# Kernel optimization log

Measured on AMD Instinct MI355X. Metric: run time of the kernel, lower is better.

The kernel has to match this reference:

```python
import jax, jax.numpy as jnp
import numpy as np

N_QUBIT = 22
N_LAYERS = 2
D_LOGICAL = 2  # num_logical_dim (one logical qubit)
DIM = 2 ** N_QUBIT


def _apply_ry(psi, th, q):
    # psi: (B, 2^n) complex64; Ry(th) on qubit q (q=0 is the most significant bit)
    half = th * 0.5
    c = jnp.cos(half).astype(jnp.complex64)
    s = jnp.sin(half).astype(jnp.complex64)
    psi4 = psi.reshape(psi.shape[0], 2 ** q, 2, -1)
    p0, p1 = psi4[:, :, 0], psi4[:, :, 1]
    out = jnp.stack([c * p0 - s * p1, s * p0 + c * p1], axis=2)
    return out.reshape(psi.shape)


def _apply_cnot(psi, c, t):
    a, b = (c, t) if c < t else (t, c)
    right = 2 ** (N_QUBIT - b - 1)
    mid = 2 ** (b - a - 1)
    psi6 = psi.reshape(psi.shape[0], 2 ** a, 2, mid, 2, right)
    if c < t:
        # control is axis 2; flip target axis 4 where control==1
        psi6 = psi6.at[:, :, 1, :, :, :].set(psi6[:, :, 1, :, ::-1, :])
    else:
        # control is axis 4; flip target axis 2 where control==1
        psi6 = psi6.at[:, :, :, :, 1, :].set(psi6[:, :, ::-1, :, 1, :])
    return psi6.reshape(psi.shape)


def _apply_pauli(psi, p, q):
    psi4 = psi.reshape(psi.shape[0], 2 ** q, 2, -1)
    p0, p1 = psi4[:, :, 0], psi4[:, :, 1]
    if p == 'X':
        out = jnp.stack([p1, p0], axis=2)
    elif p == 'Y':
        out = jnp.stack([-1j * p1, 1j * p0], axis=2)
    else:  # Z
        out = jnp.stack([p0, -p1], axis=2)
    return out.reshape(psi.shape)


def _encode(theta):
    # q0[i, i] = 1 for the logical basis states, then run the circuit
    psi = jnp.zeros((D_LOGICAL, DIM), jnp.complex64)
    psi = psi.at[jnp.arange(D_LOGICAL), jnp.arange(D_LOGICAL)].set(1.0)
    for l in range(N_LAYERS):
        for q in range(N_QUBIT):
            psi = _apply_ry(psi, theta[l, q], q)
        for q in range(N_QUBIT):
            psi = _apply_cnot(psi, q, (q + 1) % N_QUBIT)
    return psi


def _kl_loss(theta):
    psi = _encode(theta)  # (D_LOGICAL, 2^n)
    # Knill-Laflamme inner products T_e[i,j] = <psi_i| E_e |psi_j> for all weight-1 Paulis
    Ts = []
    for q in range(N_QUBIT):
        for p in ('X', 'Y', 'Z'):
            epsi = _apply_pauli(psi, p, q)
            Ts.append(jnp.einsum('is,js->ij', psi.conj(), epsi))
    T = jnp.stack(Ts)  # (3*N_QUBIT, D_LOGICAL, D_LOGICAL)
    diag = jnp.diagonal(T, axis1=1, axis2=2)
    lam = diag.mean(axis=1)  # per-error lambda_e
    res = T - lam[:, None, None] * jnp.eye(D_LOGICAL, dtype=T.dtype)
    # loss_type == 'L2'
    return jnp.sum(jnp.abs(res) ** 2)


def setup_inputs() -> dict:
    key = jax.random.key(0)
    theta = jax.random.normal(key, (N_LAYERS, N_QUBIT), dtype=jnp.float32)
    return {"theta": theta}


def reference(theta):
    return _kl_loss(theta)
```

## Files before the change

### kernel.cpp

```cpp
#include <hip/hip_runtime.h>

#define NQ 22
#define DIMN (1u << NQ)

struct MaskSet {
    unsigned L[NQ];
    unsigned Linv[NQ];
    unsigned xm[NQ];
    unsigned zm[NQ];
    unsigned frowHi[5];
};

constexpr MaskSet buildMasks() {
    MaskSet M{};
    for (int b = 0; b < NQ; ++b) M.L[b] = 1u << b;
    for (int q = 0; q < NQ; ++q) {
        int bc = NQ - 1 - q, bt = NQ - 1 - ((q + 1) % NQ);
        M.L[bt] ^= M.L[bc];
    }
    unsigned mat[NQ] = {}, aug[NQ] = {};
    for (int b = 0; b < NQ; ++b) { mat[b] = M.L[b]; aug[b] = 1u << b; }
    for (int col = 0; col < NQ; ++col) {
        int piv = col;
        while (!((mat[piv] >> col) & 1u)) ++piv;
        unsigned tm = mat[piv]; mat[piv] = mat[col]; mat[col] = tm;
        unsigned ta = aug[piv]; aug[piv] = aug[col]; aug[col] = ta;
        for (int r = 0; r < NQ; ++r)
            if (r != col && ((mat[r] >> col) & 1u)) { mat[r] ^= mat[col]; aug[r] ^= aug[col]; }
    }
    for (int b = 0; b < NQ; ++b) M.Linv[b] = aug[b];
    for (int j = 0; j < NQ; ++j) {
        int b = NQ - 1 - j;
        unsigned xmv = 0;
        for (int r = 0; r < NQ; ++r)
            if ((aug[r] >> b) & 1u) xmv |= 1u << r;
        M.xm[j] = xmv;
        M.zm[j] = M.L[b];
    }
    for (int j = 0; j < 5; ++j) {
        unsigned f = 0;
        for (int r = 0; r < NQ; ++r)
            if ((aug[r] >> (17 + j)) & 1u) f |= 1u << r;
        M.frowHi[j] = f;
    }
    return M;
}
constexpr int topbit_c(unsigned v) { int b = 0; while (v >> (b + 1)) ++b; return b; }
constexpr unsigned unionHi() {
    MaskSet M = buildMasks();
    unsigned u = 0;
    for (int j = 0; j < 5; ++j) u |= M.frowHi[j];
    return u;
}
static_assert((unionHi() & 0xFFFFu) == 0, "frowHi must only touch bits 16..21");

__device__ __forceinline__ float wave_sum(float v) {
    v += __shfl_down(v, 32); v += __shfl_down(v, 16); v += __shfl_down(v, 8);
    v += __shfl_down(v, 4);  v += __shfl_down(v, 2);  v += __shfl_down(v, 1);
    return v;
}
__device__ __forceinline__ float fflip(float v, unsigned sbit31) {
    return __int_as_float(__float_as_int(v) ^ (int)sbit31);
}
__device__ __forceinline__ unsigned ph4(unsigned g) { return g ^ ((g >> 6) & 3u); }

__global__ __launch_bounds__(256) void k_prep(const float* __restrict__ theta,
                                              float* __restrict__ acc,
                                              float* __restrict__ trig) {
    int t = threadIdx.x;
    acc[t] = 0.f;
    if (t < 2 * NQ) {
        int l = t / NQ, q = t % NQ, b = NQ - 1 - q;
        float h = 0.5f * theta[t];
        trig[l * 2 * NQ + b]      = cosf(h);
        trig[l * 2 * NQ + NQ + b] = sinf(h);
    }
}

__global__ __launch_bounds__(256, 1) void k_genHi(float* __restrict__ phi,
                                                  const float* __restrict__ trig,
                                                  float* __restrict__ acc) {
    constexpr MaskSet M = buildMasks();
    __shared__ float red[4 * 12];
    unsigned base = blockIdx.x * 256u + threadIdx.x;
    unsigned P0 = 0;
#pragma unroll
    for (int b = 0; b < NQ; ++b)
        P0 |= ((unsigned)__popc(base & M.Linv[b]) & 1u) << b;
    float pc = 1.f;
#pragma unroll
    for (int b = 1; b < 16; ++b) {
        float cvb = trig[b], svb = trig[NQ + b];
        pc *= ((P0 >> b) & 1u) ? svb : cvb;
    }
    float cv0 = trig[0], sv0 = trig[NQ];
    float C0 = pc * ((P0 & 1u) ? sv0 : cv0);
    float C1 = pc * ((P0 & 1u) ? cv0 : -sv0);
    float cb[6], sb[6];
#pragma unroll
    for (int k = 0; k < 6; ++k) { cb[k] = trig[16 + k]; sb[k] = trig[NQ + 16 + k]; }
    unsigned u0 = P0 >> 16;
    float v0[32], v1[32];
#pragma unroll
    for (int e = 0; e < 32; ++e) {
        unsigned F = 0;
        if (e & 1)  F ^= M.frowHi[0];
        if (e & 2)  F ^= M.frowHi[1];
        if (e & 4)  F ^= M.frowHi[2];
        if (e & 8)  F ^= M.frowHi[3];
        if (e & 16) F ^= M.frowHi[4];
        unsigned u = u0 ^ (F >> 16);
        float vp = (u & 1u) ? sb[0] : cb[0];
#pragma unroll
        for (int k = 1; k < 6; ++k) vp *= ((u >> k) & 1u) ? sb[k] : cb[k];
        v0[e] = vp * C0;
        v1[e] = vp * C1;
    }
    float c2[5], s2[5];
#pragma unroll
    for (int j = 0; j < 5; ++j) {
        c2[j] = trig[2 * NQ + 17 + j];
        s2[j] = trig[3 * NQ + 17 + j];
    }
#pragma unroll
    for (int j = 0; j < 5; ++j) {
#pragma unroll
        for (int e = 0; e < 32; ++e) {
            if (!(e & (1 << j))) {
                int e1 = e | (1 << j);
                float a0 = v0[e], a1 = v0[e1];
                v0[e]  = c2[j] * a0 - s2[j] * a1;
                v0[e1] = s2[j] * a0 + c2[j] * a1;
                float b0 = v1[e], b1 = v1[e1];
                v1[e]  = c2[j] * b0 - s2[j] * b1;
                v1[e1] = s2[j] * b0 + c2[j] * b1;
            }
        }
    }
#pragma unroll
    for (int e = 0; e < 32; ++e) {
        unsigned a = base | ((unsigned)e << 17);
        phi[a] = v0[e];
        phi[DIMN + a] = v1[e];
    }
    int lane = threadIdx.x & 63, w = threadIdx.x >> 6;
#pragma unroll
    for (int i = 1; i <= 3; ++i) {
        unsigned ex  = M.xm[i] >> 17;
        unsigned zme = M.zm[i] >> 17;
        float t00 = 0.f, t11 = 0.f, t01 = 0.f, u01 = 0.f;
#pragma unroll
        for (int e = 0; e < 32; ++e) {
            int ep = e ^ (int)ex;
            t00 += v0[e] * v0[ep];
            t11 += v1[e] * v1[ep];
            float p = v0[e] * v1[ep];
            t01 += p;
            unsigned sg = ((unsigned)__popc((unsigned)ep & zme) & 1u) << 31;
            u01 += fflip(p, sg);
        }
        float vals[4] = { t00, t11, t01, u01 };
#pragma unroll
        for (int j = 0; j < 4; ++j) {
            float v = wave_sum(vals[j]);
            if (lane == 0) red[w * 12 + (i - 1) * 4 + j] = v;
        }
    }
    __syncthreads();
    int t = threadIdx.x;
    if (t < 12) {
        float r = red[t] + red[12 + t] + red[24 + t] + red[36 + t];
        atomicAdd(&acc[4 + t], r);
    }
}

__global__ __launch_bounds__(256, 1) void k_midA(float* __restrict__ phi,
                                                 const float* __restrict__ trig,
                                                 float* __restrict__ acc) {
    constexpr MaskSet M = buildMasks();
    __shared__ float red[4 * 16];
    unsigned tid = blockIdx.x * 256u + threadIdx.x;
    unsigned base = (tid & 0xFFFu) | ((tid >> 12) << 17);
    float v0[32], v1[32];
#pragma unroll
    for (int e = 0; e < 32; ++e) {
        unsigned a = base | ((unsigned)e << 12);
        v0[e] = phi[a];
        v1[e] = phi[DIMN + a];
    }
    float c[5], s[5];
#pragma unroll
    for (int j = 0; j < 5; ++j) {
        c[j] = trig[2 * NQ + 12 + j];
        s[j] = trig[3 * NQ + 12 + j];
    }
#pragma unroll
    for (int j = 0; j < 5; ++j) {
#pragma unroll
        for (int e = 0; e < 32; ++e) {
            if (!(e & (1 << j))) {
                int e1 = e | (1 << j);
                float a0 = v0[e], a1 = v0[e1];
                v0[e]  = c[j] * a0 - s[j] * a1;
                v0[e1] = s[j] * a0 + c[j] * a1;
                float b0 = v1[e], b1 = v1[e1];
                v1[e]  = c[j] * b0 - s[j] * b1;
                v1[e1] = s[j] * b0 + c[j] * b1;
            }
        }
    }
#pragma unroll
    for (int e = 0; e < 32; ++e) {
        unsigned a = base | ((unsigned)e << 12);
        phi[a] = v0[e];
        phi[DIMN + a] = v1[e];
    }
    int lane = threadIdx.x & 63, w = threadIdx.x >> 6;
#pragma unroll
    for (int i = 5; i <= 8; ++i) {
        unsigned ex  = (M.xm[i] >> 12) & 31u;
        unsigned zme = (M.zm[i] >> 12) & 31u;
        unsigned bs31 = ((unsigned)__popc(base & M.zm[i]) & 1u) << 31;
        float t00 = 0.f, t11 = 0.f, t01 = 0.f, u01 = 0.f;
#pragma unroll
        for (int e = 0; e < 32; ++e) {
            int ep = e ^ (int)ex;
            t00 += v0[e] * v0[ep];
            t11 += v1[e] * v1[ep];
            float p = v0[e] * v1[ep];
            t01 += p;
            unsigned sg = ((unsigned)__popc((unsigned)ep & zme) & 1u) << 31;
            u01 += fflip(p, sg ^ bs31);
        }
        float vals[4] = { t00, t11, t01, u01 };
#pragma unroll
        for (int j = 0; j < 4; ++j) {
            float v = wave_sum(vals[j]);
            if (lane == 0) red[w * 16 + (i - 5) * 4 + j] = v;
        }
    }
    __syncthreads();
    int t = threadIdx.x;
    if (t < 16) {
        float r = red[t] + red[16 + t] + red[32 + t] + red[48 + t];
        atomicAdd(&acc[20 + t], r);
    }
}

__global__ __launch_bounds__(256) void k_low(float* __restrict__ phi,
                                             const float* __restrict__ trig,
                                             float* __restrict__ acc) {
    constexpr MaskSet M = buildMasks();
    __shared__ float As[4096];
    __shared__ float Bs[4096];
    __shared__ float red[4 * 44];
    float4* As4 = (float4*)As;
    float4* Bs4 = (float4*)Bs;
    int t = threadIdx.x;
    unsigned base = blockIdx.x * 4096u;
    float a[16], b[16];

    {
        const float4* g0 = (const float4*)(phi + base);
        const float4* g1 = (const float4*)(phi + DIMN + base);
#pragma unroll
        for (int k = 0; k < 4; ++k) {
            float4 va = g0[4 * t + k];
            a[4 * k] = va.x; a[4 * k + 1] = va.y; a[4 * k + 2] = va.z; a[4 * k + 3] = va.w;
            float4 vb = g1[4 * t + k];
            b[4 * k] = vb.x; b[4 * k + 1] = vb.y; b[4 * k + 2] = vb.z; b[4 * k + 3] = vb.w;
        }
#pragma unroll
        for (int g = 0; g < 4; ++g) {
            float c = trig[2 * NQ + g], s = trig[3 * NQ + g];
#pragma unroll
            for (int e = 0; e < 16; ++e) {
                if (!(e & (1 << g))) {
                    int e1 = e | (1 << g);
                    float x0 = a[e], x1 = a[e1];
                    a[e] = c * x0 - s * x1; a[e1] = s * x0 + c * x1;
                    float y0 = b[e], y1 = b[e1];
                    b[e] = c * y0 - s * y1; b[e1] = s * y0 + c * y1;
                }
            }
        }
        unsigned sw = (unsigned)(t >> 4) & 3u;
#pragma unroll
        for (int k = 0; k < 4; ++k) {
            unsigned f = ((unsigned)(4 * t + k)) ^ sw;
            As4[f] = make_float4(a[4 * k], a[4 * k + 1], a[4 * k + 2], a[4 * k + 3]);
            Bs4[f] = make_float4(b[4 * k], b[4 * k + 1], b[4 * k + 2], b[4 * k + 3]);
        }
    }
    __syncthreads();

    {
        unsigned lo = (unsigned)t & 15u, hi = (unsigned)t >> 4;
        unsigned swz = (hi & 3u) << 2;
#pragma unroll
        for (int j = 0; j < 16; ++j) {
            unsigned i = lo | ((unsigned)j << 4) | (hi << 8);
            a[j] = As[i ^ swz];
            b[j] = Bs[i ^ swz];
        }
#pragma unroll
        for (int g = 0; g < 4; ++g) {
            float c = trig[2 * NQ + 4 + g], s = trig[3 * NQ + 4 + g];
#pragma unroll
            for (int e = 0; e < 16; ++e) {
                if (!(e & (1 << g))) {
                    int e1 = e | (1 << g);
                    float x0 = a[e], x1 = a[e1];
                    a[e] = c * x0 - s * x1; a[e1] = s * x0 + c * x1;
                    float y0 = b[e], y1 = b[e1];
                    b[e] = c * y0 - s * y1; b[e1] = s * y0 + c * y1;
                }
            }
        }
#pragma unroll
        for (int j = 0; j < 16; ++j) {
            unsigned i = lo | ((unsigned)j << 4) | (hi << 8);
            As[i ^ swz] = a[j];
            Bs[i ^ swz] = b[j];
        }
    }
    __syncthreads();

    {
#pragma unroll
        for (int j = 0; j < 16; ++j) {
            unsigned i = (unsigned)t | ((unsigned)j << 8);
            unsigned p = i ^ (((unsigned)j & 3u) << 2);
            a[j] = As[p];
            b[j] = Bs[p];
        }
#pragma unroll
        for (int g = 0; g < 4; ++g) {
            float c = trig[2 * NQ + 8 + g], s = trig[3 * NQ + 8 + g];
#pragma unroll
            for (int e = 0; e < 16; ++e) {
                if (!(e & (1 << g))) {
                    int e1 = e | (1 << g);
                    float x0 = a[e], x1 = a[e1];
                    a[e] = c * x0 - s * x1; a[e1] = s * x0 + c * x1;
                    float y0 = b[e], y1 = b[e1];
                    b[e] = c * y0 - s * y1; b[e1] = s * y0 + c * y1;
                }
            }
        }
#pragma unroll
        for (int j = 0; j < 16; ++j) {
            unsigned i = (unsigned)t | ((unsigned)j << 8);
            phi[base + i] = a[j];
            phi[DIMN + base + i] = b[j];
            unsigned p = i ^ (((unsigned)j & 3u) << 2);
            As[p] = a[j];
            Bs[p] = b[j];
        }
    }

    float SSv[3], z0v[3], z1v[3], z2v[3], d4v[3];
    {
#pragma unroll
        for (int c = 0; c < 3; ++c) {
            float p[16];
#pragma unroll
            for (int j = 0; j < 16; ++j)
                p[j] = (c == 0) ? a[j] * a[j] : (c == 1) ? b[j] * b[j] : a[j] * b[j];
            float s1[8], d1[8];
#pragma unroll
            for (int j = 0; j < 8; ++j) { s1[j] = p[j] + p[j + 8]; d1[j] = p[j] - p[j + 8]; }
            float s2[4], d2[4];
#pragma unroll
            for (int j = 0; j < 4; ++j) { s2[j] = s1[j] + s1[j + 4]; d2[j] = d1[j] - d1[j + 4]; }
            float d3a = d2[0] - d2[2], d3b = d2[1] - d2[3];
            SSv[c] = (s2[0] + s2[1]) + (s2[2] + s2[3]);
            z0v[c] = ((d1[0] + d1[1]) + (d1[2] + d1[3])) + ((d1[4] + d1[5]) + (d1[6] + d1[7]));
            z1v[c] = (d2[0] + d2[1]) + (d2[2] + d2[3]);
            z2v[c] = d3a + d3b;
            d4v[c] = d3a - d3b;
        }
    }
    {
        unsigned Wt = (unsigned)t;
        Wt ^= Wt >> 1; Wt ^= Wt >> 2; Wt ^= Wt >> 4;
        int lane = t & 63, w = t >> 6;
#pragma unroll
        for (int c = 0; c < 3; ++c) {
            float v;
            v = wave_sum(SSv[c]); if (lane == 0) red[w * 39 + c] = v;
            v = wave_sum(z0v[c]); if (lane == 0) red[w * 39 + 3 + c] = v;
            v = wave_sum(z1v[c]); if (lane == 0) red[w * 39 + 6 + c] = v;
            v = wave_sum(z2v[c]); if (lane == 0) red[w * 39 + 9 + c] = v;
            v = wave_sum(d4v[c]); if (lane == 0) red[w * 39 + 12 + c] = v;
#pragma unroll
            for (int k = 4; k < 12; ++k) {
                unsigned sb = ((Wt >> (11 - k)) & 1u) << 31;
                v = wave_sum(fflip(d4v[c], sb));
                if (lane == 0) red[w * 39 + 3 + 3 * k + c] = v;
            }
        }
    }
    __syncthreads();
    if (t < 66) {
        int c = t % 3, q = t / 3;
        int slot = (q == 0 || q == 21) ? (3 + 33 + c) : (q < 10 ? c : 3 + 3 * (q - 10) + c);
        float val = red[slot] + red[39 + slot] + red[78 + slot] + red[117 + slot];
        unsigned sg = (unsigned)__popc(base & M.zm[q]) & 1u;
        atomicAdd(&acc[4 * NQ + 3 * q + c], sg ? -val : val);
    }
    __syncthreads();

    int lane = t & 63, w = t >> 6;

#pragma unroll
    for (int i = 0; i < 3; ++i) {
        constexpr int qn0 = 10;
        unsigned je  = (M.xm[qn0 + i] >> 8) & 15u;
        unsigned zmj = (M.zm[qn0 + i] >> 8) & 15u;
        unsigned zb31 = ((unsigned)__popc(base & M.zm[qn0 + i]) & 1u) << 31;
        float t00 = 0.f, t11 = 0.f, t01 = 0.f, u01 = 0.f;
#pragma unroll
        for (int j = 0; j < 16; ++j) {
            int jp = j ^ (int)je;
            t00 += a[j] * a[jp];
            t11 += b[j] * b[jp];
            float p = a[j] * b[jp];
            t01 += p;
            unsigned sg = ((unsigned)__popc((unsigned)jp & zmj) & 1u) << 31;
            u01 += fflip(p, sg ^ zb31);
        }
        float vals[4] = { t00, t11, t01, u01 };
#pragma unroll
        for (int j = 0; j < 4; ++j) {
            float v = wave_sum(vals[j]);
            if (lane == 0) red[w * 44 + 4 * i + j] = v;
        }
    }

#pragma unroll
    for (int i = 3; i < 11; ++i) {
        unsigned m = M.xm[10 + i], zm = M.zm[10 + i];
        unsigned zb = (unsigned)__popc(base & zm) & 1u;
        float t00 = 0.f, t11 = 0.f, t01 = 0.f, u01 = 0.f;
        if (i < 10) {
            int gb = topbit_c(M.xm[10 + i]) - 2;
            unsigned mg4 = m >> 2;
            unsigned swap2 = m & 3u;
#pragma unroll
            for (int r = 0; r < 2; ++r) {
                unsigned gc = (unsigned)t + 256u * r;
                unsigned g = ((gc >> gb) << (gb + 1)) | (gc & ((1u << gb) - 1u));
                unsigned gx = g ^ mg4;
                float4 a0 = As4[ph4(g)],  a1 = Bs4[ph4(g)];
                float4 b0 = As4[ph4(gx)], b1 = Bs4[ph4(gx)];
                if (swap2) {
                    b0 = make_float4(b0.z, b0.w, b0.x, b0.y);
                    b1 = make_float4(b1.z, b1.w, b1.x, b1.y);
                }
                unsigned szg = ((unsigned)__popc((g << 2) & zm) + zb) & 1u;
                unsigned szx = ((unsigned)__popc((gx << 2) & zm) + zb) & 1u;
                unsigned fg = szg << 31, fx = szx << 31;
                const float* A0 = &a0.x; const float* A1 = &a1.x;
                const float* B0 = &b0.x; const float* B1 = &b1.x;
#pragma unroll
                for (int j = 0; j < 4; ++j) {
                    t00 += A0[j] * B0[j];
                    t11 += A1[j] * B1[j];
                    float p = A0[j] * B1[j], r2 = B0[j] * A1[j];
                    t01 += p + r2;
                    u01 += fflip(p, fx) + fflip(r2, fg);
                }
            }
            t00 *= 2.f; t11 *= 2.f;
        } else {
#pragma unroll
            for (int k = 0; k < 4; ++k) {
                unsigned g = (unsigned)t + 256u * k;
                float4 a0 = As4[ph4(g)], a1 = Bs4[ph4(g)];
                unsigned szg = ((unsigned)__popc((g << 2) & zm) + zb) & 1u;
                const float* A0 = &a0.x; const float* A1 = &a1.x;
#pragma unroll
                for (int j = 0; j < 4; ++j) {
                    int jx = j ^ 3;
                    float p = A0[j] * A0[jx];
                    float q2 = A1[j] * A1[jx];
                    float cr = A0[j] * A1[jx];
                    t00 += p; t11 += q2; t01 += cr;
                    unsigned sj = ((unsigned)(jx >> 1) & 1u) ^ szg;
                    u01 += fflip(cr, sj << 31);
                }
            }
        }
        float vals[4] = { t00, t11, t01, u01 };
#pragma unroll
        for (int j = 0; j < 4; ++j) {
            float v = wave_sum(vals[j]);
            if (lane == 0) red[w * 44 + 4 * i + j] = v;
        }
    }
    __syncthreads();
    if (t < 44) {
        float r = red[t] + red[44 + t] + red[88 + t] + red[132 + t];
        atomicAdd(&acc[40 + t], r);
    }
}

struct Meas4Arg { unsigned xm[4]; unsigned zm[4]; int gbit[4]; int qn[4]; };

__global__ __launch_bounds__(256) void k_measS(const float* __restrict__ phi,
                                               float* __restrict__ acc,
                                               Meas4Arg M) {
    __shared__ float red[16];
    int t = threadIdx.x;
    int slice = blockIdx.y;
    unsigned m = M.xm[slice], zm = M.zm[slice];
    int gb = M.gbit[slice];
    unsigned mg4 = m >> 2;
    unsigned ml2 = m & 3u;
    unsigned zl = zm & 3u;
    unsigned pg31[4], px31[4];
#pragma unroll
    for (int j = 0; j < 4; ++j) {
        pg31[j] = (((unsigned)__popc((unsigned)j & zl) & 1u) << 31);
        px31[j] = (((unsigned)__popc(((unsigned)j ^ ml2) & zl) & 1u) << 31);
    }
    unsigned tid = blockIdx.x * 256u + (unsigned)t;
    const float4* p0 = (const float4*)phi;
    const float4* p1 = (const float4*)(phi + DIMN);
    float t00 = 0.f, t11 = 0.f, t01 = 0.f, u01 = 0.f;
#pragma unroll
    for (int it = 0; it < 8; ++it) {
        unsigned gc = tid + (unsigned)it * 65536u;
        unsigned g = ((gc >> gb) << (gb + 1)) | (gc & ((1u << gb) - 1u));
        unsigned gx = g ^ mg4;
        float4 a0 = p0[g], a1 = p1[g];
        float4 b0 = p0[gx], b1 = p1[gx];
        if (ml2) {
            b0 = make_float4(b0.y, b0.x, b0.w, b0.z);
            b1 = make_float4(b1.y, b1.x, b1.w, b1.z);
        }
        unsigned fg = (((unsigned)__popc((g << 2) & zm) & 1u) << 31);
        unsigned fx = (((unsigned)__popc((gx << 2) & zm) & 1u) << 31);
        const float* A0 = &a0.x; const float* A1 = &a1.x;
        const float* B0 = &b0.x; const float* B1 = &b1.x;
#pragma unroll
        for (int j = 0; j < 4; ++j) {
            t00 += A0[j] * B0[j];
            t11 += A1[j] * B1[j];
            float p = A0[j] * B1[j], r = B0[j] * A1[j];
            t01 += p + r;
            u01 += fflip(p, fx ^ px31[j]) + fflip(r, fg ^ pg31[j]);
        }
    }
    t00 *= 2.f; t11 *= 2.f;
    int lane = t & 63, w = t >> 6;
    float vals[4] = { t00, t11, t01, u01 };
#pragma unroll
    for (int j = 0; j < 4; ++j) {
        float v = wave_sum(vals[j]);
        if (lane == 0) red[w * 4 + j] = v;
    }
    __syncthreads();
    if (t < 4) {
        float r = red[t] + red[4 + t] + red[8 + t] + red[12 + t];
        atomicAdd(&acc[4 * M.qn[slice] + t], r);
    }
}

__global__ __launch_bounds__(64) void k_final(const float* __restrict__ acc,
                                              float* __restrict__ out) {
    int t = threadIdx.x;
    float v = 0.f;
    if (t < NQ) {
        float t00 = acc[4 * t], t11 = acc[4 * t + 1];
        float t01 = acc[4 * t + 2], u01 = acc[4 * t + 3];
        float d = t00 - t11;
        v = 0.5f * d * d + 2.f * t01 * t01 + 2.f * u01 * u01;
    } else if (t < 2 * NQ) {
        int q = t - NQ;
        float z0 = acc[4 * NQ + 3 * q], z1 = acc[4 * NQ + 3 * q + 1];
        float zz = acc[4 * NQ + 3 * q + 2];
        float d = z0 - z1;
        v = 0.5f * d * d + 2.f * zz * zz;
    }
    v += __shfl_down(v, 32); v += __shfl_down(v, 16); v += __shfl_down(v, 8);
    v += __shfl_down(v, 4);  v += __shfl_down(v, 2);  v += __shfl_down(v, 1);
    if (t == 0) out[0] = v;
}

extern "C" void kernel_launch(void* const* d_in, const int* in_sizes, int n_in,
                              void* d_out, int out_size, void* d_ws, size_t ws_size,
                              hipStream_t stream) {
    const float* theta = (const float*)d_in[0];
    float* out  = (float*)d_out;
    float* ws   = (float*)d_ws;
    float* phi  = ws;
    float* acc  = ws + 2 * (size_t)DIMN;
    float* trig = acc + 256;

    constexpr MaskSet M = buildMasks();

    Meas4Arg m4;
    const int qs[4] = { 0, 4, 9, 21 };
    for (int i = 0; i < 4; ++i) {
        int q = qs[i];
        m4.xm[i] = M.xm[q]; m4.zm[i] = M.zm[q];
        m4.gbit[i] = topbit_c(M.xm[q]) - 2;
        m4.qn[i] = q;
    }

    k_prep<<<1, 256, 0, stream>>>(theta, acc, trig);
    k_genHi<<<512, 256, 0, stream>>>(phi, trig, acc);
    k_midA<<<512, 256, 0, stream>>>(phi, trig, acc);
    k_low<<<1024, 256, 0, stream>>>(phi, trig, acc);
    k_measS<<<dim3(256, 4), 256, 0, stream>>>(phi, acc, m4);
    k_final<<<1, 64, 0, stream>>>(acc, out);
}
```

Measured before the change: 163.4 us.

## Fuse four slice measurements into one orbit-based pass over the state

Replaces the per-slice measurement kernel, which read the state four times (once per qubit slice), with a single kernel. Each thread loads an 8-element orbit generated by three XOR masks and computes all four qubits' inner products from registers. The aim is to cut global memory traffic for the measurement stage by reusing loaded amplitudes across slices. In exchange it needs more registers per thread (64 floats of loaded data), and it depends on compile-time checks that the orbit structure holds.

```diff
diff --git a/kernel.cpp b/kernel.cpp
--- a/kernel.cpp
+++ b/kernel.cpp
@@ -53,6 +53,31 @@
     return u;
 }
 static_assert((unionHi() & 0xFFFFu) == 0, "frowHi must only touch bits 16..21");
+
+constexpr unsigned orbGen(int which) {
+    MaskSet M = buildMasks();
+    return (which == 0 ? M.xm[0] : which == 1 ? M.xm[4] : M.xm[9]) >> 2;
+}
+constexpr int orbS21() {
+    MaskSet M = buildMasks();
+    unsigned GA = M.xm[0] >> 2, GB = M.xm[4] >> 2, GC = M.xm[9] >> 2;
+    unsigned GQ = M.xm[21] >> 2;
+    for (int s = 1; s < 8; ++s) {
+        unsigned c = ((s & 1) ? GA : 0u) ^ ((s & 2) ? GB : 0u) ^ ((s & 4) ? GC : 0u);
+        if (c == GQ) return s;
+    }
+    return -1;
+}
+constexpr bool orbitOK() {
+    unsigned GA = orbGen(0), GB = orbGen(1), GC = orbGen(2);
+    int cA = topbit_c(GA), cB = topbit_c(GB), cC = topbit_c(GC);
+    if (!(cC < cB && cB < cA) || cA > 19) return false;
+    if (((GA >> cB) & 1u) || ((GA >> cC) & 1u)) return false;
+    if (((GB >> cA) & 1u) || ((GB >> cC) & 1u)) return false;
+    if (((GC >> cA) & 1u) || ((GC >> cB) & 1u)) return false;
+    return orbS21() > 0;
+}
+static_assert(orbitOK(), "orbit structure for fused slice measurement must hold");
 
 __device__ __forceinline__ float wave_sum(float v) {
     v += __shfl_down(v, 32); v += __shfl_down(v, 16); v += __shfl_down(v, 8);
@@ -506,65 +531,80 @@
     }
 }
 
-struct Meas4Arg { unsigned xm[4]; unsigned zm[4]; int gbit[4]; int qn[4]; };
-
-__global__ __launch_bounds__(256) void k_measS(const float* __restrict__ phi,
-                                               float* __restrict__ acc,
-                                               Meas4Arg M) {
-    __shared__ float red[16];
-    int t = threadIdx.x;
-    int slice = blockIdx.y;
-    unsigned m = M.xm[slice], zm = M.zm[slice];
-    int gb = M.gbit[slice];
-    unsigned mg4 = m >> 2;
-    unsigned ml2 = m & 3u;
-    unsigned zl = zm & 3u;
-    unsigned pg31[4], px31[4];
-#pragma unroll
-    for (int j = 0; j < 4; ++j) {
-        pg31[j] = (((unsigned)__popc((unsigned)j & zl) & 1u) << 31);
-        px31[j] = (((unsigned)__popc(((unsigned)j ^ ml2) & zl) & 1u) << 31);
-    }
-    unsigned tid = blockIdx.x * 256u + (unsigned)t;
-    const float4* p0 = (const float4*)phi;
-    const float4* p1 = (const float4*)(phi + DIMN);
-    float t00 = 0.f, t11 = 0.f, t01 = 0.f, u01 = 0.f;
-#pragma unroll
-    for (int it = 0; it < 8; ++it) {
-        unsigned gc = tid + (unsigned)it * 65536u;
-        unsigned g = ((gc >> gb) << (gb + 1)) | (gc & ((1u << gb) - 1u));
-        unsigned gx = g ^ mg4;
-        float4 a0 = p0[g], a1 = p1[g];
-        float4 b0 = p0[gx], b1 = p1[gx];
-        if (ml2) {
-            b0 = make_float4(b0.y, b0.x, b0.w, b0.z);
-            b1 = make_float4(b1.y, b1.x, b1.w, b1.z);
-        }
-        unsigned fg = (((unsigned)__popc((g << 2) & zm) & 1u) << 31);
-        unsigned fx = (((unsigned)__popc((gx << 2) & zm) & 1u) << 31);
-        const float* A0 = &a0.x; const float* A1 = &a1.x;
-        const float* B0 = &b0.x; const float* B1 = &b1.x;
-#pragma unroll
-        for (int j = 0; j < 4; ++j) {
-            t00 += A0[j] * B0[j];
-            t11 += A1[j] * B1[j];
-            float p = A0[j] * B1[j], r = B0[j] * A1[j];
-            t01 += p + r;
-            u01 += fflip(p, fx ^ px31[j]) + fflip(r, fg ^ pg31[j]);
-        }
-    }
-    t00 *= 2.f; t11 *= 2.f;
-    int lane = t & 63, w = t >> 6;
-    float vals[4] = { t00, t11, t01, u01 };
-#pragma unroll
-    for (int j = 0; j < 4; ++j) {
-        float v = wave_sum(vals[j]);
-        if (lane == 0) red[w * 4 + j] = v;
-    }
-    __syncthreads();
-    if (t < 4) {
-        float r = red[t] + red[4 + t] + red[8 + t] + red[12 + t];
-        atomicAdd(&acc[4 * M.qn[slice] + t], r);
+__global__ __launch_bounds__(256) void k_measF(const float* __restrict__ phi,
+                                               float* __restrict__ acc) {
+    constexpr MaskSet M = buildMasks();
+    constexpr unsigned GA = orbGen(0), GB = orbGen(1), GC = orbGen(2);
+    constexpr int pc0 = topbit_c(GC), pc1 = topbit_c(GB), pc2 = topbit_c(GA);
+    __shared__ float red[4 * 16];
+    unsigned t = blockIdx.x * 256u + threadIdx.x;
+    unsigned g = t;
+    g = ((g >> pc0) << (pc0 + 1)) | (g & ((1u << pc0) - 1u));
+    g = ((g >> pc1) << (pc1 + 1)) | (g & ((1u << pc1) - 1u));
+    g = ((g >> pc2) << (pc2 + 1)) | (g & ((1u << pc2) - 1u));
+    const float4* P0 = (const float4*)phi;
+    const float4* P1 = (const float4*)(phi + DIMN);
+    unsigned idx[8];
+    float4 u4[8], w4[8];
+#pragma unroll
+    for (int s = 0; s < 8; ++s) {
+        idx[s] = g ^ ((s & 1) ? GA : 0u) ^ ((s & 2) ? GB : 0u) ^ ((s & 4) ? GC : 0u);
+        u4[s] = P0[idx[s]];
+        w4[s] = P1[idx[s]];
+    }
+    constexpr int QN[4] = { 0, 4, 9, 21 };
+    constexpr int SX[4] = { 1, 2, 4, orbS21() };
+    float res[16];
+#pragma unroll
+    for (int qi = 0; qi < 4; ++qi) {
+        const unsigned xq = M.xm[QN[qi]];
+        const unsigned zq = M.zm[QN[qi]];
+        const int sx = SX[qi];
+        const int mu = (int)(xq & 3u);
+        const unsigned zh = zq >> 2, zl = zq & 3u;
+        unsigned fz[8];
+#pragma unroll
+        for (int s = 0; s < 8; ++s)
+            fz[s] = ((unsigned)__popc(idx[s] & zh) & 1u) << 31;
+        unsigned pj31[4];
+#pragma unroll
+        for (int j = 0; j < 4; ++j)
+            pj31[j] = ((unsigned)__popc((unsigned)j & zl) & 1u) << 31;
+        float t00 = 0.f, t11 = 0.f, t01 = 0.f, u01 = 0.f;
+#pragma unroll
+        for (int s = 0; s < 8; ++s) {
+            const int s2 = s ^ sx;
+            const float* A0 = &u4[s].x;
+            const float* A1 = &w4[s].x;
+            const float* B0 = &u4[s2].x;
+            const float* B1 = &w4[s2].x;
+            const unsigned fe = fz[s2];
+#pragma unroll
+            for (int j = 0; j < 4; ++j) {
+                const int jp = j ^ mu;
+                t00 += A0[j] * B0[jp];
+                t11 += A1[j] * B1[jp];
+                float p = A0[j] * B1[jp];
+                t01 += p;
+                u01 += fflip(p, fe ^ pj31[jp]);
+            }
+        }
+        res[4 * qi + 0] = t00; res[4 * qi + 1] = t11;
+        res[4 * qi + 2] = t01; res[4 * qi + 3] = u01;
+    }
+    int lane = threadIdx.x & 63, w = threadIdx.x >> 6;
+#pragma unroll
+    for (int k = 0; k < 16; ++k) {
+        float v = wave_sum(res[k]);
+        if (lane == 0) red[w * 16 + k] = v;
+    }
+    __syncthreads();
+    int tt = threadIdx.x;
+    if (tt < 16) {
+        int qi = tt >> 2;
+        int base4 = (qi == 0) ? 0 : (qi == 1) ? 16 : (qi == 2) ? 36 : 84;
+        float r = red[tt] + red[16 + tt] + red[32 + tt] + red[48 + tt];
+        atomicAdd(&acc[base4 + (tt & 3)], r);
     }
 }
 
@@ -599,21 +639,10 @@
     float* acc  = ws + 2 * (size_t)DIMN;
     float* trig = acc + 256;
 
-    constexpr MaskSet M = buildMasks();
-
-    Meas4Arg m4;
-    const int qs[4] = { 0, 4, 9, 21 };
-    for (int i = 0; i < 4; ++i) {
-        int q = qs[i];
-        m4.xm[i] = M.xm[q]; m4.zm[i] = M.zm[q];
-        m4.gbit[i] = topbit_c(M.xm[q]) - 2;
-        m4.qn[i] = q;
-    }
-
     k_prep<<<1, 256, 0, stream>>>(theta, acc, trig);
     k_genHi<<<512, 256, 0, stream>>>(phi, trig, acc);
     k_midA<<<512, 256, 0, stream>>>(phi, trig, acc);
     k_low<<<1024, 256, 0, stream>>>(phi, trig, acc);
-    k_measS<<<dim3(256, 4), 256, 0, stream>>>(phi, acc, m4);
+    k_measF<<<512, 256, 0, stream>>>(phi, acc);
     k_final<<<1, 64, 0, stream>>>(acc, out);
 }
```

Result: slower. 169.1 us (+3.5%).
